# Kernel tuning notes

Measured on AMD Instinct MI355X. Metric: run time of the kernel, lower is better.

## Reference

```python
import jax, jax.numpy as jnp
import numpy as np
from jax import lax

B, S, I, H = 64, 512, 1024, 1024


def _lstm_dir(x, W_ih, W_hh, b_ih, b_hh):
    # x: [B, S, I] -> hidden states [B, S, H]
    # Precompute input projections for all timesteps in one GEMM.
    xg = jnp.einsum('bsi,gi->bsg', x, W_ih) + b_ih + b_hh  # [B, S, 4H]
    Whh_T = W_hh.T  # [H, 4H]
    h0 = jnp.zeros((x.shape[0], W_hh.shape[1]), dtype=x.dtype)
    c0 = jnp.zeros_like(h0)

    def step(carry, xg_t):
        h, c = carry
        g = xg_t + h @ Whh_T  # [B, 4H]
        i_g, f_g, g_g, o_g = jnp.split(g, 4, axis=-1)  # PyTorch gate order i,f,g,o
        i_g = jax.nn.sigmoid(i_g)
        f_g = jax.nn.sigmoid(f_g)
        g_g = jnp.tanh(g_g)
        o_g = jax.nn.sigmoid(o_g)
        c = f_g * c + i_g * g_g
        h = o_g * jnp.tanh(c)
        return (h, c), h

    _, hs = lax.scan(step, (h0, c0), jnp.swapaxes(xg, 0, 1))  # hs: [S, B, H]
    return jnp.swapaxes(hs, 0, 1)


def setup_inputs() -> dict:
    key = jax.random.key(0)
    ks = jax.random.split(key, 10)
    s = 1.0 / np.sqrt(H)  # PyTorch LSTMCell init scale
    return {
        'forward_x': jax.random.normal(ks[0], (B, S, I), jnp.float32),
        'backward_x': jax.random.normal(ks[1], (B, S, I), jnp.float32),
        'W_ih_f': jax.random.uniform(ks[2], (4 * H, I), jnp.float32, -s, s),
        'W_hh_f': jax.random.uniform(ks[3], (4 * H, H), jnp.float32, -s, s),
        'b_ih_f': jax.random.uniform(ks[4], (4 * H,), jnp.float32, -s, s),
        'b_hh_f': jax.random.uniform(ks[5], (4 * H,), jnp.float32, -s, s),
        'W_ih_b': jax.random.uniform(ks[6], (4 * H, I), jnp.float32, -s, s),
        'W_hh_b': jax.random.uniform(ks[7], (4 * H, H), jnp.float32, -s, s),
        'b_ih_b': jax.random.uniform(ks[8], (4 * H,), jnp.float32, -s, s),
        'b_hh_b': jax.random.uniform(ks[9], (4 * H,), jnp.float32, -s, s),
    }


def reference(forward_x, backward_x, W_ih_f, W_hh_f, b_ih_f, b_hh_f,
              W_ih_b, W_hh_b, b_ih_b, b_hh_b):
    fwd = _lstm_dir(forward_x, W_ih_f, W_hh_f, b_ih_f, b_hh_f)
    # Backward direction consumes backward_x from the last timestep to the
    # first and writes hidden states back at their original positions,
    # i.e. run on the time-reversed sequence and reverse the outputs.
    bwd = _lstm_dir(backward_x[:, ::-1, :], W_ih_b, W_hh_b, b_ih_b, b_hh_b)[:, ::-1, :]
    return fwd, bwd
```

## Files before the change

kernel.cpp:

```cpp
#include <hip/hip_runtime.h>
#include <hip/hip_bf16.h>
#include <cstdint>


typedef __bf16 bf16_t;
typedef bf16_t bf16x8 __attribute__((ext_vector_type(8)));
typedef float  f32x4  __attribute__((ext_vector_type(4)));
typedef int    i32x2  __attribute__((ext_vector_type(2)));

#define DEVI __device__ __forceinline__

constexpr int Bb = 64, Ss = 512, Ii = 1024, Hh = 1024;
constexpr size_t WS_FLAGS  = 0;
constexpr size_t WS_HRING  = 4096;
constexpr size_t WS_XBF    = 1ull << 20;
constexpr size_t XBF_BYTES = 2ull * Ss * Bb * Ii * 2;
constexpr size_t WS_NEED_XBF = WS_XBF + XBF_BYTES;
constexpr int LDS_TOTAL = 163840;

DEVI float fast_sig(float x) {
  float z = __expf(-fabsf(x));
  float r = __builtin_amdgcn_rcpf(1.f + z);
  return x >= 0.f ? r : z * r;
}
DEVI float fast_tanh(float x) {
  float z = __expf(-2.f * fabsf(x));
  float r = (1.f - z) * __builtin_amdgcn_rcpf(1.f + z);
  return x >= 0.f ? r : -r;
}
DEVI bf16x8 cvt8(f32x4 a, f32x4 b) {
  bf16x8 r;
  r[0] = (bf16_t)a[0]; r[1] = (bf16_t)a[1]; r[2] = (bf16_t)a[2]; r[3] = (bf16_t)a[3];
  r[4] = (bf16_t)b[0]; r[5] = (bf16_t)b[1]; r[6] = (bf16_t)b[2]; r[7] = (bf16_t)b[3];
  return r;
}
DEVI uint32_t pk_bf16(float lo, float hi) {
  union { bf16_t b[2]; uint32_t u; } x;
  x.b[0] = (bf16_t)lo; x.b[1] = (bf16_t)hi;
  return x.u;
}
DEVI f32x4 mfma16(bf16x8 a, bf16x8 b, f32x4 c) {
  return __builtin_amdgcn_mfma_f32_16x16x32_bf16(a, b, c, 0, 0, 0);
}

#define GLDS16(g, s)                                                           \
  __builtin_amdgcn_global_load_lds(                                            \
      (const __attribute__((address_space(1))) void*)(const void*)(g),         \
      (__attribute__((address_space(3))) void*)(void*)(s), 16, 0, 0)
#define GLDS16_COH(g, s)                                                       \
  __builtin_amdgcn_global_load_lds(                                            \
      (const __attribute__((address_space(1))) void*)(const void*)(g),         \
      (__attribute__((address_space(3))) void*)(void*)(s), 16, 0, 17)
#define WAIT_LGKM0 asm volatile("s_waitcnt lgkmcnt(0)" ::: "memory")
#define WAIT_VM0   asm volatile("s_waitcnt vmcnt(0)" ::: "memory")
#define BARRIER_RAW                                                            \
  do { __builtin_amdgcn_s_barrier(); __builtin_amdgcn_sched_barrier(0); } while (0)

__global__ void k_init(int* flags) {
  int i = threadIdx.x;
  if (i < 256) flags[i] = 0;
}

__global__ void k_convx(const float* __restrict__ xf, const float* __restrict__ xb,
                        bf16_t* __restrict__ dst) {
  size_t og = (size_t)blockIdx.x * blockDim.x + threadIdx.x;
  int i8  = (int)(og & 127);
  int b   = (int)((og >> 7) & 63);
  int t   = (int)((og >> 13) & 511);
  int dir = (int)(og >> 22);
  const float* src = (dir ? xb : xf) + (((size_t)b * Ss + t) * Ii + (size_t)i8 * 8);
  f32x4 a = *(const f32x4*)src;
  f32x4 c = *(const f32x4*)(src + 4);
  *(bf16x8*)(dst + og * 8) = cvt8(a, c);
}

template <bool XBF>
__global__ void __launch_bounds__(512, 2)
k_lstm(const float* __restrict__ xf, const float* __restrict__ xb,
       const float* __restrict__ Wih_f, const float* __restrict__ Whh_f,
       const float* __restrict__ bih_f, const float* __restrict__ bhh_f,
       const float* __restrict__ Wih_b, const float* __restrict__ Whh_b,
       const float* __restrict__ bih_b, const float* __restrict__ bhh_b,
       float* __restrict__ out,
       const bf16_t* __restrict__ xbfin, bf16_t* __restrict__ hring,
       int* __restrict__ flags) {
  extern __shared__ char lds[];
  char* PA = lds;
  char* PB = lds + 65536;
  float* part = (float*)(lds + 131072);

  const int tid = threadIdx.x;
  const int bid = blockIdx.x;
  const int dir = bid & 1;
  const int db  = bid >> 1;
  const int n0  = db * 8;
  const int w   = tid >> 6, l = tid & 63;
  const int u   = l >> 4, l15 = l & 15;
  const int m   = w & 1;
  const int kq  = w >> 1;

  const float* Wih = dir ? Wih_b : Wih_f;
  const float* Whh = dir ? Whh_b : Whh_f;
  const float* bih = dir ? bih_b : bih_f;
  const float* bhh = dir ? bhh_b : bhh_f;
  const float* x32 = dir ? xb : xf;
  const bf16_t* xbase = xbfin + (size_t)dir * Ss * Bb * Ii;
  bf16_t* hr = hring + (size_t)dir * 2 * Bb * Hh;
  float* outD = out + (size_t)dir * Bb * Ss * Hh;
  int* myflags = flags + dir * 128;

  bf16x8 wr[2][2][4][2];
#pragma unroll
  for (int mat = 0; mat < 2; ++mat)
#pragma unroll
    for (int p = 0; p < 2; ++p)
#pragma unroll
      for (int ks = 0; ks < 4; ++ks)
#pragma unroll
        for (int nt = 0; nt < 2; ++nt) {
          int c = nt * 16 + l15;
          int j = (c >> 3) * 1024 + n0 + (c & 7);
          int k = p * 512 + kq * 128 + ks * 32 + u * 8;
          const float* sp = (mat ? Whh : Wih) + (size_t)j * 1024 + k;
          wr[mat][p][ks][nt] = cvt8(*(const f32x4*)sp, *(const f32x4*)(sp + 4));
        }

  const int eb = tid >> 3, en = tid & 7;
  const int nj = n0 + en;
  float bi0 = bih[nj] + bhh[nj];
  float bi1 = bih[1024 + nj] + bhh[1024 + nj];
  float bi2 = bih[2048 + nj] + bhh[2048 + nj];
  float bi3 = bih[3072 + nj] + bhh[3072 + nj];

  int aoff0[4], aoff1[4];
#pragma unroll
  for (int ks = 0; ks < 4; ++ks) {
    int r0 = m * 32 + l15;
    int r1 = r0 + 16;
    int sl = kq * 16 + ks * 4 + u;
    aoff0[ks] = r0 * 1024 + ((sl ^ (r0 & 7)) << 4);
    aoff1[ks] = r1 * 1024 + ((sl ^ (r1 & 7)) << 4);
  }

  auto STAGE_DMA = [&](char* panel, const bf16_t* srcb) {
#pragma unroll
    for (int i = 0; i < 8; ++i) {
      const bf16_t* gp = srcb + (size_t)(w * 8 + i) * 1024 + ((l ^ i) << 3);
      GLDS16(gp, panel + (w * 8 + i) * 1024);
    }
  };
  auto STAGE_H = [&](char* panel, const bf16_t* srcb) {
#pragma unroll
    for (int i = 0; i < 8; ++i) {
      const bf16_t* gp = srcb + (size_t)(w * 8 + i) * 1024 + ((l ^ i) << 3);
      GLDS16_COH(gp, panel + (w * 8 + i) * 1024);
    }
  };
  auto STAGE_XF = [&](char* panel, const float* srcb) {
#pragma unroll
    for (int i = 0; i < 8; ++i) {
      int r = w * 8 + i;
      const float* sp = srcb + (size_t)r * (Ss * Ii) + ((l ^ i) << 3);
      f32x4 a = *(const f32x4*)sp;
      f32x4 b = *(const f32x4*)(sp + 4);
      *(bf16x8*)(panel + r * 1024 + l * 16) = cvt8(a, b);
    }
  };

  f32x4 acc00, acc01, acc10, acc11;
#define COMPUTE(panel, matC, pC)                                               \
  do {                                                                         \
    _Pragma("unroll") for (int ks = 0; ks < 4; ++ks) {                         \
      bf16x8 a0_ = *(const bf16x8*)((panel) + aoff0[ks]);                      \
      bf16x8 a1_ = *(const bf16x8*)((panel) + aoff1[ks]);                      \
      acc00 = mfma16(a0_, wr[matC][pC][ks][0], acc00);                         \
      acc01 = mfma16(a0_, wr[matC][pC][ks][1], acc01);                         \
      acc10 = mfma16(a1_, wr[matC][pC][ks][0], acc10);                         \
      acc11 = mfma16(a1_, wr[matC][pC][ks][1], acc11);                         \
    }                                                                          \
  } while (0)

  float c_reg = 0.f;

  {
    int t0 = dir ? (Ss - 1) : 0;
    if constexpr (XBF) {
      STAGE_DMA(PA, xbase + (size_t)t0 * (Bb * Ii));
      STAGE_DMA(PB, xbase + (size_t)t0 * (Bb * Ii) + 512);
    } else {
      STAGE_XF(PA, x32 + (size_t)t0 * Ii);
      STAGE_XF(PB, x32 + (size_t)t0 * Ii + 512);
    }
  }

  for (int step = 0; step < Ss; ++step) {
    const int t  = dir ? (Ss - 1 - step) : step;
    const int tn = dir ? (Ss - 2 - step) : (step + 1);
    const bf16_t* hbase = hr + (size_t)((step - 1) & 1) * (Bb * Hh);

    WAIT_VM0; WAIT_LGKM0; BARRIER_RAW;

    acc00 = f32x4{0.f, 0.f, 0.f, 0.f}; acc01 = acc00; acc10 = acc00; acc11 = acc00;

    COMPUTE(PA, 0, 0);
    COMPUTE(PB, 0, 1);
    WAIT_LGKM0;

    if (step > 0 && w == 0) {
      const int* fp = &myflags[l * 2];
      for (;;) {
        i32x2 f;
        asm volatile("global_load_dwordx2 %0, %1, off sc0 sc1\n\t"
                     "s_waitcnt vmcnt(0)"
                     : "=v"(f) : "v"((uint64_t)fp) : "memory");
        if (__ballot((f[0] < step) || (f[1] < step)) == 0ull) break;
        __builtin_amdgcn_s_sleep(1);
      }
    }
    BARRIER_RAW;

    if (step > 0) {
      STAGE_H(PA, hbase);
      STAGE_H(PB, hbase + 512);
      WAIT_VM0; BARRIER_RAW;
      COMPUTE(PA, 1, 0);
      COMPUTE(PB, 1, 1);
      WAIT_LGKM0;
    }

#pragma unroll
    for (int rr = 0; rr < 2; ++rr)
#pragma unroll
      for (int nt = 0; nt < 2; ++nt) {
        f32x4 a = (rr == 0) ? (nt == 0 ? acc00 : acc01) : (nt == 0 ? acc10 : acc11);
#pragma unroll
        for (int q = 0; q < 4; ++q) {
          int R = m * 32 + rr * 16 + u * 4 + q;
          int C = nt * 16 + l15;
          part[(kq * 64 + R) * 32 + (C ^ ((R & 7) << 2))] = a[q];
        }
      }
    WAIT_LGKM0; BARRIER_RAW;

    float hval;
    {
      const int sk = (eb & 7) << 2;
      float g0 = bi0, g1 = bi1, g2 = bi2, g3 = bi3;
#pragma unroll
      for (int q = 0; q < 4; ++q) {
        const float* pp = &part[(q * 64 + eb) * 32];
        g0 += pp[en ^ sk]; g1 += pp[(8 + en) ^ sk];
        g2 += pp[(16 + en) ^ sk]; g3 += pp[(24 + en) ^ sk];
      }
      float ig = fast_sig(g0), fg = fast_sig(g1);
      float gg = fast_tanh(g2), og = fast_sig(g3);
      c_reg = fg * c_reg + ig * gg;
      hval = og * fast_tanh(c_reg);
      uint32_t p01 = pk_bf16(hval, __shfl_xor(hval, 1));
      uint32_t p23 = __shfl_xor(p01, 2);
      if ((en & 3) == 0) {
        uint64_t q8 = (uint64_t)p01 | ((uint64_t)p23 << 32);
        uint64_t* dst = (uint64_t*)&hr[(size_t)(step & 1) * (Bb * Hh) +
                                       (size_t)eb * Hh + n0 + (en & 4)];
        __hip_atomic_store(dst, q8, __ATOMIC_RELAXED, __HIP_MEMORY_SCOPE_AGENT);
      }
    }

    WAIT_VM0; BARRIER_RAW;
    if (tid == 0) {
      __hip_atomic_store(&myflags[db], step + 1, __ATOMIC_RELAXED,
                         __HIP_MEMORY_SCOPE_AGENT);
    }

    outD[(size_t)eb * (Ss * Hh) + (size_t)t * Hh + n0 + en] = hval;
    if (step < Ss - 1) {
      if constexpr (XBF) {
        STAGE_DMA(PA, xbase + (size_t)tn * (Bb * Ii));
        STAGE_DMA(PB, xbase + (size_t)tn * (Bb * Ii) + 512);
      } else {
        STAGE_XF(PA, x32 + (size_t)tn * Ii);
        STAGE_XF(PB, x32 + (size_t)tn * Ii + 512);
      }
    }
  }
#undef COMPUTE
}

extern "C" void kernel_launch(void* const* d_in, const int* in_sizes, int n_in,
                              void* d_out, int out_size, void* d_ws, size_t ws_size,
                              hipStream_t stream) {
  (void)in_sizes; (void)n_in; (void)out_size;
  const float* xf    = (const float*)d_in[0];
  const float* xb    = (const float*)d_in[1];
  const float* Wih_f = (const float*)d_in[2];
  const float* Whh_f = (const float*)d_in[3];
  const float* bih_f = (const float*)d_in[4];
  const float* bhh_f = (const float*)d_in[5];
  const float* Wih_b = (const float*)d_in[6];
  const float* Whh_b = (const float*)d_in[7];
  const float* bih_b = (const float*)d_in[8];
  const float* bhh_b = (const float*)d_in[9];
  float* outp = (float*)d_out;
  char* ws = (char*)d_ws;
  int* flagsp = (int*)(ws + WS_FLAGS);
  bf16_t* hringp = (bf16_t*)(ws + WS_HRING);
  const bf16_t* xbfp = (const bf16_t*)(ws + WS_XBF);
  const bool use_xbf = ws_size >= WS_NEED_XBF;

  hipLaunchKernelGGL(k_init, dim3(1), dim3(256), 0, stream, flagsp);
  if (use_xbf) {
    hipLaunchKernelGGL(k_convx, dim3(32768), dim3(256), 0, stream,
                       xf, xb, (bf16_t*)(ws + WS_XBF));
  }

  void* args[] = {&xf, &xb, &Wih_f, &Whh_f, &bih_f, &bhh_f,
                  &Wih_b, &Whh_b, &bih_b, &bhh_b,
                  &outp, &xbfp, &hringp, &flagsp};
  using KFn = void (*)(const float*, const float*, const float*, const float*,
                       const float*, const float*, const float*, const float*,
                       const float*, const float*, float*, const bf16_t*,
                       bf16_t*, int*);
  KFn kp = use_xbf ? (KFn)k_lstm<true> : (KFn)k_lstm<false>;
  hipFuncSetAttribute((const void*)kp, hipFuncAttributeMaxDynamicSharedMemorySize,
                      LDS_TOTAL);
  hipLaunchCooperativeKernel((const void*)kp, dim3(256), dim3(512), args,
                             LDS_TOTAL, stream);
}
```

Measured before the change: 3.712 ms.

## Speculatively poll step flags during input GEMM and split h staging

The flag check for the previous step's hidden state is issued as an asynchronous load before the first input-projection half, and its result is shared through LDS. If all producers are already done, the first half of h is staged while the second input half computes, and the recurrent compute is split so the first half starts after a partial vmcnt wait. If producers are not done, it falls back to a per-thread atomic spin-wait. The hidden-state output store is also moved before the flag publish. This adds control-flow complexity and relies on the exact vmcnt count matching the staged load count.

```diff
diff --git a/kernel.cpp b/kernel.cpp
--- a/kernel.cpp
+++ b/kernel.cpp
@@ -52,7 +52,8 @@
       (const __attribute__((address_space(1))) void*)(const void*)(g),         \
       (__attribute__((address_space(3))) void*)(void*)(s), 16, 0, 17)
 #define WAIT_LGKM0 asm volatile("s_waitcnt lgkmcnt(0)" ::: "memory")
-#define WAIT_VM0   asm volatile("s_waitcnt vmcnt(0)" ::: "memory")
+#define WAIT_VM(n) asm volatile("s_waitcnt vmcnt(" #n ")" ::: "memory")
+#define WAIT_VM0   WAIT_VM(0)
 #define BARRIER_RAW                                                            \
   do { __builtin_amdgcn_s_barrier(); __builtin_amdgcn_sched_barrier(0); } while (0)
 
@@ -202,30 +203,51 @@
 
     acc00 = f32x4{0.f, 0.f, 0.f, 0.f}; acc01 = acc00; acc10 = acc00; acc11 = acc00;
 
+    i32x2 fsw;
+    const bool sweep = (step > 0) && (w == 0);
+    if (sweep) {
+      asm volatile("global_load_dwordx2 %0, %1, off sc0 sc1"
+                   : "=v"(fsw) : "v"((uint64_t)&myflags[l * 2]) : "memory");
+    }
     COMPUTE(PA, 0, 0);
+    if (sweep) {
+      __builtin_amdgcn_sched_barrier(0);
+      asm volatile("s_waitcnt vmcnt(0)" : "+v"(fsw) :: "memory");
+      int bad = (fsw[0] < step) || (fsw[1] < step);
+      int allok = (__ballot(bad) == 0ull) ? 1 : 0;
+      if (l == 0) ((volatile int*)part)[0] = allok;
+    }
+    WAIT_LGKM0; BARRIER_RAW;
+    const int ok = (step > 0) ? ((volatile int*)part)[0] : 0;
+
+    if (ok) STAGE_H(PA, hbase);
     COMPUTE(PB, 0, 1);
-    WAIT_LGKM0;
-
-    if (step > 0 && w == 0) {
-      const int* fp = &myflags[l * 2];
-      for (;;) {
-        i32x2 f;
-        asm volatile("global_load_dwordx2 %0, %1, off sc0 sc1\n\t"
-                     "s_waitcnt vmcnt(0)"
-                     : "=v"(f) : "v"((uint64_t)fp) : "memory");
-        if (__ballot((f[0] < step) || (f[1] < step)) == 0ull) break;
-        __builtin_amdgcn_s_sleep(1);
-      }
-    }
-    BARRIER_RAW;
+    WAIT_LGKM0; BARRIER_RAW;
 
     if (step > 0) {
-      STAGE_H(PA, hbase);
-      STAGE_H(PB, hbase + 512);
-      WAIT_VM0; BARRIER_RAW;
-      COMPUTE(PA, 1, 0);
-      COMPUTE(PB, 1, 1);
-      WAIT_LGKM0;
+      if (ok) {
+        STAGE_H(PB, hbase + 512);
+        WAIT_VM(8); BARRIER_RAW;
+        COMPUTE(PA, 1, 0);
+        WAIT_LGKM0;
+        WAIT_VM0; BARRIER_RAW;
+        COMPUTE(PB, 1, 1);
+        WAIT_LGKM0;
+      } else {
+        if (tid < 128) {
+          const int* fp = &myflags[tid];
+          while (__hip_atomic_load(fp, __ATOMIC_RELAXED,
+                                   __HIP_MEMORY_SCOPE_AGENT) < step) {
+          }
+        }
+        BARRIER_RAW;
+        STAGE_H(PA, hbase);
+        STAGE_H(PB, hbase + 512);
+        WAIT_VM0; BARRIER_RAW;
+        COMPUTE(PA, 1, 0);
+        COMPUTE(PB, 1, 1);
+        WAIT_LGKM0;
+      }
     }
 
 #pragma unroll
@@ -242,7 +264,6 @@
       }
     WAIT_LGKM0; BARRIER_RAW;
 
-    float hval;
     {
       const int sk = (eb & 7) << 2;
       float g0 = bi0, g1 = bi1, g2 = bi2, g3 = bi3;
@@ -255,8 +276,9 @@
       float ig = fast_sig(g0), fg = fast_sig(g1);
       float gg = fast_tanh(g2), og = fast_sig(g3);
       c_reg = fg * c_reg + ig * gg;
-      hval = og * fast_tanh(c_reg);
-      uint32_t p01 = pk_bf16(hval, __shfl_xor(hval, 1));
+      float h = og * fast_tanh(c_reg);
+      outD[(size_t)eb * (Ss * Hh) + (size_t)t * Hh + n0 + en] = h;
+      uint32_t p01 = pk_bf16(h, __shfl_xor(h, 1));
       uint32_t p23 = __shfl_xor(p01, 2);
       if ((en & 3) == 0) {
         uint64_t q8 = (uint64_t)p01 | ((uint64_t)p23 << 32);
@@ -272,7 +294,6 @@
                          __HIP_MEMORY_SCOPE_AGENT);
     }
 
-    outD[(size_t)eb * (Ss * Hh) + (size_t)t * Hh + n0 + en] = hval;
     if (step < Ss - 1) {
       if constexpr (XBF) {
         STAGE_DMA(PA, xbase + (size_t)tn * (Bb * Ii));
```

Result: slower. 4.034 ms (+8.7%).

## Use per-wave private LDS slabs to drop barriers and the bf16 x pre-conversion

Applied to the files above, without the earlier changes.

Each wave now stages only the A-operand rows it consumes into its own 16KB LDS slab, so the workgroup barriers around x and h staging are removed. The flag spin loses its s_sleep, the h DMA is split into two vmcnt waits so the first half's MFMAs can start before the second half arrives, and the separate x fp32-to-bf16 conversion kernel is dropped in favour of converting inline from fp32 each step. The intent is to shorten the serial per-step critical path. In exchange, x is read as fp32 with direct loads every step, and intra-wave LDS reuse depends on each wave waiting correctly on its own writes.

```diff
diff --git a/kernel.cpp b/kernel.cpp
--- a/kernel.cpp
+++ b/kernel.cpp
@@ -11,11 +11,8 @@
 #define DEVI __device__ __forceinline__
 
 constexpr int Bb = 64, Ss = 512, Ii = 1024, Hh = 1024;
-constexpr size_t WS_FLAGS  = 0;
-constexpr size_t WS_HRING  = 4096;
-constexpr size_t WS_XBF    = 1ull << 20;
-constexpr size_t XBF_BYTES = 2ull * Ss * Bb * Ii * 2;
-constexpr size_t WS_NEED_XBF = WS_XBF + XBF_BYTES;
+constexpr size_t WS_FLAGS = 0;
+constexpr size_t WS_HRING = 4096;
 constexpr int LDS_TOTAL = 163840;
 
 DEVI float fast_sig(float x) {
@@ -43,38 +40,19 @@
   return __builtin_amdgcn_mfma_f32_16x16x32_bf16(a, b, c, 0, 0, 0);
 }
 
-#define GLDS16(g, s)                                                           \
-  __builtin_amdgcn_global_load_lds(                                            \
-      (const __attribute__((address_space(1))) void*)(const void*)(g),         \
-      (__attribute__((address_space(3))) void*)(void*)(s), 16, 0, 0)
 #define GLDS16_COH(g, s)                                                       \
   __builtin_amdgcn_global_load_lds(                                            \
       (const __attribute__((address_space(1))) void*)(const void*)(g),         \
       (__attribute__((address_space(3))) void*)(void*)(s), 16, 0, 17)
 #define WAIT_LGKM0 asm volatile("s_waitcnt lgkmcnt(0)" ::: "memory")
-#define WAIT_VM0   asm volatile("s_waitcnt vmcnt(0)" ::: "memory")
+#define WAIT_VM(n) asm volatile("s_waitcnt vmcnt(" #n ")" ::: "memory")
 #define BARRIER_RAW                                                            \
   do { __builtin_amdgcn_s_barrier(); __builtin_amdgcn_sched_barrier(0); } while (0)
 
 __global__ void k_init(int* flags) {
-  int i = threadIdx.x;
-  if (i < 256) flags[i] = 0;
-}
-
-__global__ void k_convx(const float* __restrict__ xf, const float* __restrict__ xb,
-                        bf16_t* __restrict__ dst) {
-  size_t og = (size_t)blockIdx.x * blockDim.x + threadIdx.x;
-  int i8  = (int)(og & 127);
-  int b   = (int)((og >> 7) & 63);
-  int t   = (int)((og >> 13) & 511);
-  int dir = (int)(og >> 22);
-  const float* src = (dir ? xb : xf) + (((size_t)b * Ss + t) * Ii + (size_t)i8 * 8);
-  f32x4 a = *(const f32x4*)src;
-  f32x4 c = *(const f32x4*)(src + 4);
-  *(bf16x8*)(dst + og * 8) = cvt8(a, c);
-}
-
-template <bool XBF>
+  if (threadIdx.x < 256) flags[threadIdx.x] = 0;
+}
+
 __global__ void __launch_bounds__(512, 2)
 k_lstm(const float* __restrict__ xf, const float* __restrict__ xb,
        const float* __restrict__ Wih_f, const float* __restrict__ Whh_f,
@@ -82,13 +60,8 @@
        const float* __restrict__ Wih_b, const float* __restrict__ Whh_b,
        const float* __restrict__ bih_b, const float* __restrict__ bhh_b,
        float* __restrict__ out,
-       const bf16_t* __restrict__ xbfin, bf16_t* __restrict__ hring,
-       int* __restrict__ flags) {
+       bf16_t* __restrict__ hring, int* __restrict__ flags) {
   extern __shared__ char lds[];
-  char* PA = lds;
-  char* PB = lds + 65536;
-  float* part = (float*)(lds + 131072);
-
   const int tid = threadIdx.x;
   const int bid = blockIdx.x;
   const int dir = bid & 1;
@@ -99,12 +72,14 @@
   const int m   = w & 1;
   const int kq  = w >> 1;
 
+  char* slab = lds + w * 16384;
+  float* part = (float*)(lds + 131072);
+
   const float* Wih = dir ? Wih_b : Wih_f;
   const float* Whh = dir ? Whh_b : Whh_f;
   const float* bih = dir ? bih_b : bih_f;
   const float* bhh = dir ? bhh_b : bhh_f;
   const float* x32 = dir ? xb : xf;
-  const bf16_t* xbase = xbfin + (size_t)dir * Ss * Bb * Ii;
   bf16_t* hr = hring + (size_t)dir * 2 * Bb * Hh;
   float* outD = out + (size_t)dir * Bb * Ss * Hh;
   int* myflags = flags + dir * 128;
@@ -132,47 +107,42 @@
   float bi2 = bih[2048 + nj] + bhh[2048 + nj];
   float bi3 = bih[3072 + nj] + bhh[3072 + nj];
 
-  int aoff0[4], aoff1[4];
-#pragma unroll
-  for (int ks = 0; ks < 4; ++ks) {
-    int r0 = m * 32 + l15;
-    int r1 = r0 + 16;
-    int sl = kq * 16 + ks * 4 + u;
-    aoff0[ks] = r0 * 1024 + ((sl ^ (r0 & 7)) << 4);
-    aoff1[ks] = r1 * 1024 + ((sl ^ (r1 & 7)) << 4);
-  }
-
-  auto STAGE_DMA = [&](char* panel, const bf16_t* srcb) {
-#pragma unroll
-    for (int i = 0; i < 8; ++i) {
-      const bf16_t* gp = srcb + (size_t)(w * 8 + i) * 1024 + ((l ^ i) << 3);
-      GLDS16(gp, panel + (w * 8 + i) * 1024);
-    }
+  int sw[4];
+#pragma unroll
+  for (int ks = 0; ks < 4; ++ks) sw[ks] = (((ks * 4 + u) ^ l15) << 4);
+  const int ro0 = l15 * 256, ro1 = (l15 + 16) * 256;
+
+  auto DMA_H = [&](const bf16_t* hb) {
+#pragma unroll
+    for (int p = 0; p < 2; ++p)
+#pragma unroll
+      for (int i = 0; i < 8; ++i) {
+        int sr = i * 4 + u;
+        const bf16_t* gp = hb + (size_t)(m * 32 + sr) * 1024 + p * 512 +
+                           kq * 128 + ((l15 ^ (sr & 15)) << 3);
+        GLDS16_COH(gp, slab + p * 8192 + i * 1024);
+      }
   };
-  auto STAGE_H = [&](char* panel, const bf16_t* srcb) {
-#pragma unroll
-    for (int i = 0; i < 8; ++i) {
-      const bf16_t* gp = srcb + (size_t)(w * 8 + i) * 1024 + ((l ^ i) << 3);
-      GLDS16_COH(gp, panel + (w * 8 + i) * 1024);
-    }
+  auto STAGE_X = [&](int tt) {
+#pragma unroll
+    for (int p = 0; p < 2; ++p)
+#pragma unroll
+      for (int i = 0; i < 8; ++i) {
+        int sr = i * 4 + u;
+        const float* sp = x32 + ((size_t)(m * 32 + sr) * Ss + tt) * Ii +
+                          p * 512 + kq * 128 + ((l15 ^ (sr & 15)) << 3);
+        f32x4 a = *(const f32x4*)sp;
+        f32x4 b2 = *(const f32x4*)(sp + 4);
+        *(bf16x8*)(slab + p * 8192 + i * 1024 + l * 16) = cvt8(a, b2);
+      }
   };
-  auto STAGE_XF = [&](char* panel, const float* srcb) {
-#pragma unroll
-    for (int i = 0; i < 8; ++i) {
-      int r = w * 8 + i;
-      const float* sp = srcb + (size_t)r * (Ss * Ii) + ((l ^ i) << 3);
-      f32x4 a = *(const f32x4*)sp;
-      f32x4 b = *(const f32x4*)(sp + 4);
-      *(bf16x8*)(panel + r * 1024 + l * 16) = cvt8(a, b);
-    }
-  };
 
   f32x4 acc00, acc01, acc10, acc11;
-#define COMPUTE(panel, matC, pC)                                               \
+#define COMP(matC, pC)                                                         \
   do {                                                                         \
     _Pragma("unroll") for (int ks = 0; ks < 4; ++ks) {                         \
-      bf16x8 a0_ = *(const bf16x8*)((panel) + aoff0[ks]);                      \
-      bf16x8 a1_ = *(const bf16x8*)((panel) + aoff1[ks]);                      \
+      bf16x8 a0_ = *(const bf16x8*)(slab + (pC) * 8192 + ro0 + sw[ks]);        \
+      bf16x8 a1_ = *(const bf16x8*)(slab + (pC) * 8192 + ro1 + sw[ks]);        \
       acc00 = mfma16(a0_, wr[matC][pC][ks][0], acc00);                         \
       acc01 = mfma16(a0_, wr[matC][pC][ks][1], acc01);                         \
       acc10 = mfma16(a1_, wr[matC][pC][ks][0], acc10);                         \
@@ -182,50 +152,35 @@
 
   float c_reg = 0.f;
 
-  {
-    int t0 = dir ? (Ss - 1) : 0;
-    if constexpr (XBF) {
-      STAGE_DMA(PA, xbase + (size_t)t0 * (Bb * Ii));
-      STAGE_DMA(PB, xbase + (size_t)t0 * (Bb * Ii) + 512);
-    } else {
-      STAGE_XF(PA, x32 + (size_t)t0 * Ii);
-      STAGE_XF(PB, x32 + (size_t)t0 * Ii + 512);
-    }
-  }
+  STAGE_X(dir ? (Ss - 1) : 0);
 
   for (int step = 0; step < Ss; ++step) {
     const int t  = dir ? (Ss - 1 - step) : step;
     const int tn = dir ? (Ss - 2 - step) : (step + 1);
     const bf16_t* hbase = hr + (size_t)((step - 1) & 1) * (Bb * Hh);
 
-    WAIT_VM0; WAIT_LGKM0; BARRIER_RAW;
-
     acc00 = f32x4{0.f, 0.f, 0.f, 0.f}; acc01 = acc00; acc10 = acc00; acc11 = acc00;
-
-    COMPUTE(PA, 0, 0);
-    COMPUTE(PB, 0, 1);
-    WAIT_LGKM0;
-
-    if (step > 0 && w == 0) {
-      const int* fp = &myflags[l * 2];
-      for (;;) {
-        i32x2 f;
-        asm volatile("global_load_dwordx2 %0, %1, off sc0 sc1\n\t"
-                     "s_waitcnt vmcnt(0)"
-                     : "=v"(f) : "v"((uint64_t)fp) : "memory");
-        if (__ballot((f[0] < step) || (f[1] < step)) == 0ull) break;
-        __builtin_amdgcn_s_sleep(1);
-      }
-    }
-    BARRIER_RAW;
+    COMP(0, 0);
+    COMP(0, 1);
 
     if (step > 0) {
-      STAGE_H(PA, hbase);
-      STAGE_H(PB, hbase + 512);
-      WAIT_VM0; BARRIER_RAW;
-      COMPUTE(PA, 1, 0);
-      COMPUTE(PB, 1, 1);
-      WAIT_LGKM0;
+      if (w == 0) {
+        const int* fp = &myflags[l * 2];
+        for (;;) {
+          i32x2 f;
+          asm volatile("global_load_dwordx2 %0, %1, off sc0 sc1\n\t"
+                       "s_waitcnt vmcnt(0)"
+                       : "=v"(f) : "v"((uint64_t)fp) : "memory");
+          if (__ballot((f[0] < step) || (f[1] < step)) == 0ull) break;
+        }
+      }
+      BARRIER_RAW;
+
+      DMA_H(hbase);
+      WAIT_VM(8);
+      COMP(1, 0);
+      WAIT_VM(0);
+      COMP(1, 1);
     }
 
 #pragma unroll
@@ -265,31 +220,22 @@
         __hip_atomic_store(dst, q8, __ATOMIC_RELAXED, __HIP_MEMORY_SCOPE_AGENT);
       }
     }
-
-    WAIT_VM0; BARRIER_RAW;
+    WAIT_VM(0); BARRIER_RAW;
     if (tid == 0) {
       __hip_atomic_store(&myflags[db], step + 1, __ATOMIC_RELAXED,
                          __HIP_MEMORY_SCOPE_AGENT);
     }
 
     outD[(size_t)eb * (Ss * Hh) + (size_t)t * Hh + n0 + en] = hval;
-    if (step < Ss - 1) {
-      if constexpr (XBF) {
-        STAGE_DMA(PA, xbase + (size_t)tn * (Bb * Ii));
-        STAGE_DMA(PB, xbase + (size_t)tn * (Bb * Ii) + 512);
-      } else {
-        STAGE_XF(PA, x32 + (size_t)tn * Ii);
-        STAGE_XF(PB, x32 + (size_t)tn * Ii + 512);
-      }
-    }
+    if (step < Ss - 1) STAGE_X(tn);
   }
-#undef COMPUTE
+#undef COMP
 }
 
 extern "C" void kernel_launch(void* const* d_in, const int* in_sizes, int n_in,
                               void* d_out, int out_size, void* d_ws, size_t ws_size,
                               hipStream_t stream) {
-  (void)in_sizes; (void)n_in; (void)out_size;
+  (void)in_sizes; (void)n_in; (void)out_size; (void)ws_size;
   const float* xf    = (const float*)d_in[0];
   const float* xb    = (const float*)d_in[1];
   const float* Wih_f = (const float*)d_in[2];
@@ -304,23 +250,15 @@
   char* ws = (char*)d_ws;
   int* flagsp = (int*)(ws + WS_FLAGS);
   bf16_t* hringp = (bf16_t*)(ws + WS_HRING);
-  const bf16_t* xbfp = (const bf16_t*)(ws + WS_XBF);
-  const bool use_xbf = ws_size >= WS_NEED_XBF;
 
   hipLaunchKernelGGL(k_init, dim3(1), dim3(256), 0, stream, flagsp);
-  if (use_xbf) {
-    hipLaunchKernelGGL(k_convx, dim3(32768), dim3(256), 0, stream,
-                       xf, xb, (bf16_t*)(ws + WS_XBF));
-  }
 
   void* args[] = {&xf, &xb, &Wih_f, &Whh_f, &bih_f, &bhh_f,
                   &Wih_b, &Whh_b, &bih_b, &bhh_b,
-                  &outp, &xbfp, &hringp, &flagsp};
-  using KFn = void (*)(const float*, const float*, const float*, const float*,
-                       const float*, const float*, const float*, const float*,
-                       const float*, const float*, float*, const bf16_t*,
-                       bf16_t*, int*);
-  KFn kp = use_xbf ? (KFn)k_lstm<true> : (KFn)k_lstm<false>;
+                  &outp, &hringp, &flagsp};
+  void (*kp)(const float*, const float*, const float*, const float*,
+             const float*, const float*, const float*, const float*,
+             const float*, const float*, float*, bf16_t*, int*) = k_lstm;
   hipFuncSetAttribute((const void*)kp, hipFuncAttributeMaxDynamicSharedMemorySize,
                       LDS_TOTAL);
   hipLaunchCooperativeKernel((const void*)kp, dim3(256), dim3(512), args,
```

Result: slower. 6.420 ms (+73.0%).

## Stage h per-warp into private LDS slabs and drop the block barrier before recurrent MFMA

Applied to the files above, without the earlier changes.

Each warp now DMAs only the slice of the previous hidden state it needs into its own LDS slab. It splits the wait (vmcnt 8, then 0) so the first half's MFMAs start while the second half is still loading, and it removes the block-wide barrier between the h load and the recurrent compute. The flag wait now has 128 threads each spin on one flag, with no sleep, in place of a single warp polling pairs with backoff. The output store moves before the inter-block flag publish, so it is covered by the existing vmcnt wait. This targets the serial per-step latency on the recurrent critical path. The risks are more polling traffic and the slab overlapping PA/PB panel memory, which could race with x staging.

```diff
diff --git a/kernel.cpp b/kernel.cpp
--- a/kernel.cpp
+++ b/kernel.cpp
@@ -6,7 +6,6 @@
 typedef __bf16 bf16_t;
 typedef bf16_t bf16x8 __attribute__((ext_vector_type(8)));
 typedef float  f32x4  __attribute__((ext_vector_type(4)));
-typedef int    i32x2  __attribute__((ext_vector_type(2)));
 
 #define DEVI __device__ __forceinline__
 
@@ -52,7 +51,9 @@
       (const __attribute__((address_space(1))) void*)(const void*)(g),         \
       (__attribute__((address_space(3))) void*)(void*)(s), 16, 0, 17)
 #define WAIT_LGKM0 asm volatile("s_waitcnt lgkmcnt(0)" ::: "memory")
-#define WAIT_VM0   asm volatile("s_waitcnt vmcnt(0)" ::: "memory")
+#define WAIT_VM(n)                                                             \
+  do { asm volatile("s_waitcnt vmcnt(" #n ")" ::: "memory");                   \
+       __builtin_amdgcn_sched_barrier(0); } while (0)
 #define BARRIER_RAW                                                            \
   do { __builtin_amdgcn_s_barrier(); __builtin_amdgcn_sched_barrier(0); } while (0)
 
@@ -99,6 +100,8 @@
   const int m   = w & 1;
   const int kq  = w >> 1;
 
+  char* slab = lds + w * 16384;
+
   const float* Wih = dir ? Wih_b : Wih_f;
   const float* Whh = dir ? Whh_b : Whh_f;
   const float* bih = dir ? bih_b : bih_f;
@@ -141,19 +144,16 @@
     aoff0[ks] = r0 * 1024 + ((sl ^ (r0 & 7)) << 4);
     aoff1[ks] = r1 * 1024 + ((sl ^ (r1 & 7)) << 4);
   }
+  int hsw[4];
+#pragma unroll
+  for (int ks = 0; ks < 4; ++ks) hsw[ks] = (((ks * 4 + u) ^ (l15 & 12)) << 4);
+  const int hro0 = l15 * 256, hro1 = (l15 + 16) * 256;
 
   auto STAGE_DMA = [&](char* panel, const bf16_t* srcb) {
 #pragma unroll
     for (int i = 0; i < 8; ++i) {
       const bf16_t* gp = srcb + (size_t)(w * 8 + i) * 1024 + ((l ^ i) << 3);
       GLDS16(gp, panel + (w * 8 + i) * 1024);
-    }
-  };
-  auto STAGE_H = [&](char* panel, const bf16_t* srcb) {
-#pragma unroll
-    for (int i = 0; i < 8; ++i) {
-      const bf16_t* gp = srcb + (size_t)(w * 8 + i) * 1024 + ((l ^ i) << 3);
-      GLDS16_COH(gp, panel + (w * 8 + i) * 1024);
     }
   };
   auto STAGE_XF = [&](char* panel, const float* srcb) {
@@ -166,17 +166,41 @@
       *(bf16x8*)(panel + r * 1024 + l * 16) = cvt8(a, b);
     }
   };
+  const int u4 = l >> 4, g16 = l & 15;
+  auto DMA_H = [&](const bf16_t* hb) {
+#pragma unroll
+    for (int p = 0; p < 2; ++p)
+#pragma unroll
+      for (int j = 0; j < 8; ++j) {
+        int r = j * 4 + u4;
+        int sg = g16 ^ (r & 12);
+        const bf16_t* gp = hb + (size_t)(m * 32 + r) * 1024 + p * 512 +
+                           kq * 128 + sg * 8;
+        GLDS16_COH(gp, slab + p * 8192 + j * 1024);
+      }
+  };
 
   f32x4 acc00, acc01, acc10, acc11;
-#define COMPUTE(panel, matC, pC)                                               \
+#define COMPX(panel, pC)                                                       \
   do {                                                                         \
     _Pragma("unroll") for (int ks = 0; ks < 4; ++ks) {                         \
       bf16x8 a0_ = *(const bf16x8*)((panel) + aoff0[ks]);                      \
       bf16x8 a1_ = *(const bf16x8*)((panel) + aoff1[ks]);                      \
-      acc00 = mfma16(a0_, wr[matC][pC][ks][0], acc00);                         \
-      acc01 = mfma16(a0_, wr[matC][pC][ks][1], acc01);                         \
-      acc10 = mfma16(a1_, wr[matC][pC][ks][0], acc10);                         \
-      acc11 = mfma16(a1_, wr[matC][pC][ks][1], acc11);                         \
+      acc00 = mfma16(a0_, wr[0][pC][ks][0], acc00);                            \
+      acc01 = mfma16(a0_, wr[0][pC][ks][1], acc01);                            \
+      acc10 = mfma16(a1_, wr[0][pC][ks][0], acc10);                            \
+      acc11 = mfma16(a1_, wr[0][pC][ks][1], acc11);                            \
+    }                                                                          \
+  } while (0)
+#define COMPH(pC)                                                              \
+  do {                                                                         \
+    _Pragma("unroll") for (int ks = 0; ks < 4; ++ks) {                         \
+      bf16x8 a0_ = *(const bf16x8*)(slab + (pC) * 8192 + hro0 + hsw[ks]);      \
+      bf16x8 a1_ = *(const bf16x8*)(slab + (pC) * 8192 + hro1 + hsw[ks]);      \
+      acc00 = mfma16(a0_, wr[1][pC][ks][0], acc00);                            \
+      acc01 = mfma16(a0_, wr[1][pC][ks][1], acc01);                            \
+      acc10 = mfma16(a1_, wr[1][pC][ks][0], acc10);                            \
+      acc11 = mfma16(a1_, wr[1][pC][ks][1], acc11);                            \
     }                                                                          \
   } while (0)
 
@@ -198,33 +222,27 @@
     const int tn = dir ? (Ss - 2 - step) : (step + 1);
     const bf16_t* hbase = hr + (size_t)((step - 1) & 1) * (Bb * Hh);
 
-    WAIT_VM0; WAIT_LGKM0; BARRIER_RAW;
+    WAIT_VM(0); WAIT_LGKM0; BARRIER_RAW;
 
     acc00 = f32x4{0.f, 0.f, 0.f, 0.f}; acc01 = acc00; acc10 = acc00; acc11 = acc00;
 
-    COMPUTE(PA, 0, 0);
-    COMPUTE(PB, 0, 1);
+    COMPX(PA, 0);
+    COMPX(PB, 1);
     WAIT_LGKM0;
 
-    if (step > 0 && w == 0) {
-      const int* fp = &myflags[l * 2];
-      for (;;) {
-        i32x2 f;
-        asm volatile("global_load_dwordx2 %0, %1, off sc0 sc1\n\t"
-                     "s_waitcnt vmcnt(0)"
-                     : "=v"(f) : "v"((uint64_t)fp) : "memory");
-        if (__ballot((f[0] < step) || (f[1] < step)) == 0ull) break;
-        __builtin_amdgcn_s_sleep(1);
+    if (step > 0 && tid < 128) {
+      const int* fp = &myflags[tid];
+      while (__hip_atomic_load(fp, __ATOMIC_RELAXED, __HIP_MEMORY_SCOPE_AGENT) < step) {
       }
     }
     BARRIER_RAW;
 
     if (step > 0) {
-      STAGE_H(PA, hbase);
-      STAGE_H(PB, hbase + 512);
-      WAIT_VM0; BARRIER_RAW;
-      COMPUTE(PA, 1, 0);
-      COMPUTE(PB, 1, 1);
+      DMA_H(hbase);
+      WAIT_VM(8);
+      COMPH(0);
+      WAIT_VM(0);
+      COMPH(1);
       WAIT_LGKM0;
     }
 
@@ -242,7 +260,6 @@
       }
     WAIT_LGKM0; BARRIER_RAW;
 
-    float hval;
     {
       const int sk = (eb & 7) << 2;
       float g0 = bi0, g1 = bi1, g2 = bi2, g3 = bi3;
@@ -255,8 +272,9 @@
       float ig = fast_sig(g0), fg = fast_sig(g1);
       float gg = fast_tanh(g2), og = fast_sig(g3);
       c_reg = fg * c_reg + ig * gg;
-      hval = og * fast_tanh(c_reg);
-      uint32_t p01 = pk_bf16(hval, __shfl_xor(hval, 1));
+      float h = og * fast_tanh(c_reg);
+      outD[(size_t)eb * (Ss * Hh) + (size_t)t * Hh + n0 + en] = h;
+      uint32_t p01 = pk_bf16(h, __shfl_xor(h, 1));
       uint32_t p23 = __shfl_xor(p01, 2);
       if ((en & 3) == 0) {
         uint64_t q8 = (uint64_t)p01 | ((uint64_t)p23 << 32);
@@ -266,13 +284,12 @@
       }
     }
 
-    WAIT_VM0; BARRIER_RAW;
+    WAIT_VM(0); BARRIER_RAW;
     if (tid == 0) {
       __hip_atomic_store(&myflags[db], step + 1, __ATOMIC_RELAXED,
                          __HIP_MEMORY_SCOPE_AGENT);
     }
 
-    outD[(size_t)eb * (Ss * Hh) + (size_t)t * Hh + n0 + en] = hval;
     if (step < Ss - 1) {
       if constexpr (XBF) {
         STAGE_DMA(PA, xbase + (size_t)tn * (Bb * Ii));
@@ -283,7 +300,8 @@
       }
     }
   }
-#undef COMPUTE
+#undef COMPX
+#undef COMPH
 }
 
 extern "C" void kernel_launch(void* const* d_in, const int* in_sizes, int n_in,
```

Result: slower. 4.615 ms (+24.3%).
